# Kernel tuning notes

Hardware: AMD Instinct MI355X
Metric: run time of the kernel (lower is better)

## Reference

```python
import jax, jax.numpy as jnp
import numpy as np

B, L, N, D, TOPK, OUT_V = 32, 512, 1024, 64, 20, 1024
BN_EPS = 1e-5
NEG_SLOPE = 0.2


def setup_inputs() -> dict:
    key = jax.random.key(0)
    ks = jax.random.split(key, 8)
    s = lambda k, shape, sc=0.05: jax.random.normal(k, shape, jnp.float32) * sc
    return {
        "x_enc": jax.random.normal(ks[0], (B, L, N), jnp.float32),
        "emb": s(ks[1], (N, D), 0.1),          # nn.Embedding(variate, d_model).weight
        "lin_W": s(ks[2], (L, D)),              # GraphLayer.lin (no bias)
        "att_i": s(ks[3], (D,)),
        "att_j": s(ks[4], (D,)),
        "att_em_i": s(ks[5], (D,)),
        "att_em_j": s(ks[6], (D,)),
        "gnn_b": jnp.zeros((D,), jnp.float32),  # GraphLayer bias (concat=False)
        "g1": jnp.ones((D,), jnp.float32), "b1": jnp.zeros((D,), jnp.float32),   # GNNLayer.bn
        "g2": jnp.ones((D,), jnp.float32), "b2": jnp.zeros((D,), jnp.float32),   # bn_outlayer_in
        "out_W": s(ks[7], (D, 1)), "out_b": jnp.zeros((1,), jnp.float32),        # OutLayer Linear(d_model, 1)
    }


def _forward(x_enc, emb, lin_W, att_i, att_j, att_em_i, att_em_j,
             gnn_b, g1, b1, g2, b2, out_W, out_b):
    # --- LIN: LayerNorm(input_len, eps=0, no affine) over time, first OUT_V variates ---
    xv = jnp.transpose(x_enc[:, :, :OUT_V], (0, 2, 1))          # [B, OUT_V, L]
    xv = (xv - xv.mean(-1, keepdims=True)) / jnp.sqrt(xv.var(-1, keepdims=True))
    x_enc = x_enc.at[:, :, :OUT_V].set(jnp.transpose(xv, (0, 2, 1)))
    x_enc = jnp.nan_to_num(x_enc, nan=0.0, posinf=0.0, neginf=0.0)

    gt = x_enc[:, -1:, :OUT_V]                                   # [B, 1, OUT_V]
    enc = x_enc.at[:, -1:, :OUT_V].set(0.0)

    # x = enc.transpose(0,1).view(-1, L)  (faithful to original reshape)
    x = jnp.transpose(enc, (1, 0, 2)).reshape(-1, L)             # [B*N, L]

    # --- dynamic top-k cosine-similarity graph (embeddings detached) ---
    w = jax.lax.stop_gradient(emb)
    nrm = jnp.linalg.norm(w, axis=-1)
    cos = (w @ w.T) / (nrm[:, None] * nrm[None, :])              # [N, N]
    topk_idx = jax.lax.top_k(cos, TOPK)[1]                       # [N, TOPK]
    src = topk_idx.reshape(-1)                                   # gated_j (source)
    dst = jnp.repeat(jnp.arange(N), TOPK)                        # gated_i (target)

    offs = (jnp.arange(B) * N)[:, None]
    src_b = (src[None, :] + offs).reshape(-1)                    # [B*N*TOPK]
    dst_b = (dst[None, :] + offs).reshape(-1)

    # remove_self_loops (mask out) then add_self_loops for all B*N nodes
    num_nodes = B * N
    self_mask = jnp.concatenate([src_b == dst_b, jnp.zeros(num_nodes, bool)])
    src_all = jnp.concatenate([src_b, jnp.arange(num_nodes)])
    dst_all = jnp.concatenate([dst_b, jnp.arange(num_nodes)])

    # --- GraphLayer (GAT-style, heads=1, concat=False) ---
    h = x @ lin_W                                                # [B*N, D]
    all_emb = jnp.tile(emb, (B, 1))                              # [B*N, D]

    logit = (h[dst_all] @ att_i + all_emb[dst_all] @ att_em_i
             + h[src_all] @ att_j + all_emb[src_all] @ att_em_j)  # [E]
    logit = jnp.where(logit >= 0, logit, NEG_SLOPE * logit)      # leaky_relu(0.2)
    logit = jnp.where(self_mask, -jnp.inf, logit)

    seg_max = jax.ops.segment_max(logit, dst_all, num_segments=num_nodes)
    expv = jnp.where(self_mask, 0.0, jnp.exp(logit - seg_max[dst_all]))
    denom = jax.ops.segment_sum(expv, dst_all, num_segments=num_nodes)
    alpha = expv / denom[dst_all]

    out = jax.ops.segment_sum(h[src_all] * alpha[:, None], dst_all,
                              num_segments=num_nodes) + gnn_b    # [B*N, D]

    # GNNLayer: BatchNorm1d(D) (batch stats) + ReLU
    out = (out - out.mean(0)) / jnp.sqrt(out.var(0) + BN_EPS) * g1 + b1
    out = jax.nn.relu(out)

    # --- combine with embedding, bn_outlayer_in, OutLayer ---
    xg = out.reshape(B, N, D) * emb[None]                        # [B, N, D]
    xg = jnp.transpose(xg, (0, 2, 1))                            # [B, D, N]
    mu = xg.mean((0, 2), keepdims=True)
    var = xg.var((0, 2), keepdims=True)
    xg = (xg - mu) / jnp.sqrt(var + BN_EPS) * g2[None, :, None] + b2[None, :, None]
    xg = jnp.transpose(jax.nn.relu(xg), (0, 2, 1))               # [B, N, D]

    o = xg @ out_W + out_b                                       # [B, N, 1]
    o = jnp.transpose(o, (0, 2, 1))                              # [B, 1, N]
    return o[:, :, :OUT_V], gt


def reference(x_enc, emb, lin_W, att_i, att_j, att_em_i, att_em_j,
              gnn_b, g1, b1, g2, b2, out_W, out_b):
    return _forward(x_enc, emb, lin_W, att_i, att_j, att_em_i, att_em_j,
                    gnn_b, g1, b1, g2, b2, out_W, out_b)
```

## Files before the change

### kernel.cpp

```cpp
#include <hip/hip_runtime.h>
#include <stdint.h>

#define BB 32
#define LL 512
#define NNODES 1024
#define DD 64
#define TOPK 20
#define NTOT (BB*NNODES)
#define LNSZ (LL*NNODES)

typedef short short8 __attribute__((ext_vector_type(8)));
typedef float floatx4 __attribute__((ext_vector_type(4)));

__device__ __forceinline__ float bf2f(unsigned short u){
    union { unsigned int i; float f; } x; x.i = ((unsigned int)u) << 16; return x.f;
}
__device__ __forceinline__ unsigned short f2bf(float f){
    union { float f; unsigned int i; } x; x.f = f;
    unsigned int u = x.i;
    return (unsigned short)((u + 0x7FFFu + ((u >> 16) & 1u)) >> 16);
}
__device__ __forceinline__ void unpack2(unsigned int w, float& lo, float& hi){
    union { unsigned int i; float f; } a, b;
    a.i = w << 16; b.i = w & 0xFFFF0000u;
    lo = a.f; hi = b.f;
}
__device__ __forceinline__ float ldf(const void* p, int i, int isf){
    return isf ? ((const float*)p)[i] : bf2f(((const unsigned short*)p)[i]);
}

__global__ void __launch_bounds__(256) kd_detect(const unsigned short* x, int* flag, float* stats){
    __shared__ int cnt;
    stats[threadIdx.x] = 0.f;
    if (threadIdx.x == 0) cnt = 0;
    __syncthreads();
    unsigned int idx = (threadIdx.x * 131071u) & 0x7FFFFFu;
    float v = bf2f(x[idx * 2]);
    float a = fabsf(v);
    int crazy = (!(a <= 1e3f)) || (v != 0.f && a < 1e-6f);
    atomicAdd(&cnt, crazy);
    __syncthreads();
    if (threadIdx.x == 0) flag[0] = (cnt > 64) ? 1 : 0;
}

__global__ void __launch_bounds__(256) k0_prep(const void* lw, unsigned short* wt,
                                               const void* emb, const void* aemi, const void* aemj,
                                               float* eai, float* eaj, const int* dtf){
    int isf = dtf[0];
    int id = blockIdx.x * 256 + threadIdx.x;
    int k = id >> 6, d = id & 63;
    unsigned short w = isf ? f2bf(((const float*)lw)[id]) : ((const unsigned short*)lw)[id];
    wt[d * 512 + k] = w;
    if (id < 1024){
        int n = id;
        float s1 = 0.f, s2 = 0.f;
        for (int dd = 0; dd < 64; dd++){
            float e = ldf(emb, n * 64 + dd, isf);
            s1 += e * ldf(aemi, dd, isf);
            s2 += e * ldf(aemj, dd, isf);
        }
        eai[n] = s1; eaj[n] = s2;
    }
}

__global__ void __launch_bounds__(256) k1a_partial(const void* x, float* part, const int* dtf){
    int isf = dtf[0];
    int t = threadIdx.x;
    int b = blockIdx.x >> 4, lq = blockIdx.x & 15;
    int n0 = t * 4;
    size_t base = (size_t)b * LNSZ + (size_t)(lq * 32) * NNODES + n0;
    float s0=0,s1=0,s2=0,s3=0,q0=0,q1=0,q2=0,q3=0;
    if (isf){
        const float* p = (const float*)x + base;
        for (int i = 0; i < 32; i++){
            float4 w = *(const float4*)p;
            s0+=w.x; q0+=w.x*w.x; s1+=w.y; q1+=w.y*w.y;
            s2+=w.z; q2+=w.z*w.z; s3+=w.w; q3+=w.w*w.w;
            p += NNODES;
        }
    } else {
        const unsigned short* p = (const unsigned short*)x + base;
        for (int i = 0; i < 32; i++){
            uint2 w = *(const uint2*)p;
            float a,bv,c,d2;
            unpack2(w.x, a, bv); unpack2(w.y, c, d2);
            s0+=a; q0+=a*a; s1+=bv; q1+=bv*bv; s2+=c; q2+=c*c; s3+=d2; q3+=d2*d2;
            p += NNODES;
        }
    }
    int v = b * NNODES + n0;
    float2* pp = (float2*)part;
    pp[(size_t)v*16 + lq]       = make_float2(s0,q0);
    pp[(size_t)(v+1)*16 + lq]   = make_float2(s1,q1);
    pp[(size_t)(v+2)*16 + lq]   = make_float2(s2,q2);
    pp[(size_t)(v+3)*16 + lq]   = make_float2(s3,q3);
}

__global__ void __launch_bounds__(256) k1b_finalize(const void* x, const float* part,
                                                    float* mr, float* outp, const int* dtf){
    int isf = dtf[0];
    int v = blockIdx.x * 256 + threadIdx.x;
    const float2* pp = (const float2*)part + (size_t)v * 16;
    float s = 0.f, q = 0.f;
    for (int i = 0; i < 16; i++){ float2 w = pp[i]; s += w.x; q += w.y; }
    float mean = s * (1.f/512.f);
    float var  = q * (1.f/512.f) - mean * mean;
    float rstd = var > 0.f ? rsqrtf(var) : 0.f;
    ((float2*)mr)[v] = make_float2(mean, rstd);
    int b = v >> 10, n = v & 1023;
    float xv = ldf(x, (int)((size_t)b * LNSZ + (size_t)511 * NNODES + n), isf);
    outp[NTOT + v] = (xv - mean) * rstd;
}

__global__ void __launch_bounds__(256) k2_gemm_h(const void* x, const unsigned short* wt,
                                                const float* mr, float* h, const int* dtf){
    __shared__ unsigned short A_l[128 * 136];
    __shared__ unsigned short W_l[64 * 136];
    __shared__ float4 colp4[256];
    int isf = dtf[0];
    int t = threadIdx.x;
    int q = blockIdx.x & 63, mtile = blockIdx.x >> 6;
    int b = q >> 1, nbase = (q & 1) * 512;
    size_t xbase = (size_t)b * LNSZ + nbase;

    colp4[t] = ((const float4*)mr)[q * 256 + t];

    int wave = t >> 6, lane = t & 63;
    int quad = lane >> 4, lcol = lane & 15;
    floatx4 acc[2][4];
    for (int i = 0; i < 2; i++) for (int j = 0; j < 4; j++) acc[i][j] = (floatx4){0.f,0.f,0.f,0.f};
    __syncthreads();

    for (int kc = 0; kc < 4; kc++){
        for (int i = 0; i < 8; i++){
            int id = i * 256 + t;
            int l = id >> 4, c16 = id & 15;
            int lg = mtile * 128 + l;
            uint4 o;
            if (lg == 511){
                o = make_uint4(0u, 0u, 0u, 0u);
            } else {
                size_t ofs = xbase + (size_t)lg * NNODES + kc * 128 + c16 * 8;
                float e0,e1,e2,e3,e4,e5,e6,e7;
                if (isf){
                    const float4* px = (const float4*)((const float*)x + ofs);
                    float4 wa = px[0], wb = px[1];
                    e0=wa.x; e1=wa.y; e2=wa.z; e3=wa.w; e4=wb.x; e5=wb.y; e6=wb.z; e7=wb.w;
                } else {
                    uint4 w = *(const uint4*)((const unsigned short*)x + ofs);
                    unpack2(w.x,e0,e1); unpack2(w.y,e2,e3); unpack2(w.z,e4,e5); unpack2(w.w,e6,e7);
                }
                int f4b = kc * 64 + c16 * 4;
                float4 pA = colp4[f4b+0], pB = colp4[f4b+1], pC = colp4[f4b+2], pD = colp4[f4b+3];
                e0 = (e0 - pA.x) * pA.y;  e1 = (e1 - pA.z) * pA.w;
                e2 = (e2 - pB.x) * pB.y;  e3 = (e3 - pB.z) * pB.w;
                e4 = (e4 - pC.x) * pC.y;  e5 = (e5 - pC.z) * pC.w;
                e6 = (e6 - pD.x) * pD.y;  e7 = (e7 - pD.z) * pD.w;
                o.x = (unsigned)f2bf(e0) | ((unsigned)f2bf(e1) << 16);
                o.y = (unsigned)f2bf(e2) | ((unsigned)f2bf(e3) << 16);
                o.z = (unsigned)f2bf(e4) | ((unsigned)f2bf(e5) << 16);
                o.w = (unsigned)f2bf(e6) | ((unsigned)f2bf(e7) << 16);
            }
            *(uint4*)&A_l[l * 136 + c16 * 8] = o;
        }
        for (int i = 0; i < 4; i++){
            int id = i * 256 + t;
            int dd = id >> 4, c16 = id & 15;
            uint4 w = *(const uint4*)(wt + dd * 512 + kc * 128 + c16 * 8);
            *(uint4*)&W_l[dd * 136 + c16 * 8] = w;
        }
        __syncthreads();
        for (int ks = 0; ks < 4; ks++){
            short8 af[2], bfr[4];
            af[0] = *(const short8*)&A_l[(wave * 32 + lcol) * 136 + ks * 32 + quad * 8];
            af[1] = *(const short8*)&A_l[(wave * 32 + 16 + lcol) * 136 + ks * 32 + quad * 8];
            for (int tc = 0; tc < 4; tc++)
                bfr[tc] = *(const short8*)&W_l[(tc * 16 + lcol) * 136 + ks * 32 + quad * 8];
            for (int tr = 0; tr < 2; tr++)
                for (int tc = 0; tc < 4; tc++)
                    acc[tr][tc] = __builtin_amdgcn_mfma_f32_16x16x32_bf16(af[tr], bfr[tc], acc[tr][tc], 0, 0, 0);
        }
        __syncthreads();
    }
    for (int tr = 0; tr < 2; tr++) for (int tc = 0; tc < 4; tc++){
        int dcol = tc * 16 + lcol;
        for (int r = 0; r < 4; r++){
            int lrow = wave * 32 + tr * 16 + quad * 4 + r;
            int lg = mtile * 128 + lrow;
            int row = lg * 64 + q;
            h[(size_t)row * 64 + dcol] = acc[tr][tc][r];
        }
    }
}

__global__ void __launch_bounds__(256) k3_topk(const void* emb, int* topk, const int* dtf){
    __shared__ float enf[4][64];
    int isf = dtf[0];
    int wave = threadIdx.x >> 6, lane = threadIdx.x & 63;
    int n = blockIdx.x * 4 + wave;
    float e = ldf(emb, n * 64 + lane, isf);
    enf[wave][lane] = e;
    float p1 = e * e;
    #pragma unroll
    for (int m = 1; m < 64; m <<= 1) p1 += __shfl_xor(p1, m, 64);
    __syncthreads();
    float rn_own = rsqrtf(p1);
    const float* en = enf[wave];
    float va[16];
    for (int ii = 0; ii < 16; ii++){
        int m = ii * 64 + lane;
        float dot = 0.f, sq = 0.f;
        if (isf){
            const float4* pm = (const float4*)((const float*)emb + m * 64);
            #pragma unroll
            for (int i = 0; i < 16; i++){
                float4 w = pm[i];
                dot += en[i*4+0]*w.x + en[i*4+1]*w.y + en[i*4+2]*w.z + en[i*4+3]*w.w;
                sq  += w.x*w.x + w.y*w.y + w.z*w.z + w.w*w.w;
            }
        } else {
            const uint4* pm = (const uint4*)((const unsigned short*)emb + m * 64);
            #pragma unroll
            for (int i = 0; i < 8; i++){
                uint4 w = pm[i];
                float a0,a1,a2,a3,a4,a5,a6,a7;
                unpack2(w.x,a0,a1); unpack2(w.y,a2,a3); unpack2(w.z,a4,a5); unpack2(w.w,a6,a7);
                dot += en[i*8+0]*a0 + en[i*8+1]*a1 + en[i*8+2]*a2 + en[i*8+3]*a3
                     + en[i*8+4]*a4 + en[i*8+5]*a5 + en[i*8+6]*a6 + en[i*8+7]*a7;
                sq  += a0*a0 + a1*a1 + a2*a2 + a3*a3 + a4*a4 + a5*a5 + a6*a6 + a7*a7;
            }
        }
        va[ii] = dot * rn_own * rsqrtf(sq);
    }
    for (int k = 0; k < TOPK; k++){
        float t8[8]; int x8[8];
        #pragma unroll
        for (int j = 0; j < 8; j++){
            bool c = va[2*j+1] > va[2*j];
            t8[j] = c ? va[2*j+1] : va[2*j]; x8[j] = c ? 2*j+1 : 2*j;
        }
        #pragma unroll
        for (int j = 0; j < 4; j++){
            bool c = t8[2*j+1] > t8[2*j];
            t8[j] = c ? t8[2*j+1] : t8[2*j]; x8[j] = c ? x8[2*j+1] : x8[2*j];
        }
        #pragma unroll
        for (int j = 0; j < 2; j++){
            bool c = t8[2*j+1] > t8[2*j];
            t8[j] = c ? t8[2*j+1] : t8[2*j]; x8[j] = c ? x8[2*j+1] : x8[2*j];
        }
        bool c0 = t8[1] > t8[0];
        float bv = c0 ? t8[1] : t8[0]; int bi = c0 ? x8[1] : x8[0];
        int bm = bi * 64 + lane;
        #pragma unroll
        for (int s = 1; s < 64; s <<= 1){
            float ov = __shfl_xor(bv, s, 64);
            int   om = __shfl_xor(bm, s, 64);
            bool u = (ov > bv) || (ov == bv && om < bm);
            bv = u ? ov : bv; bm = u ? om : bm;
        }
        if (lane == 0) topk[n * TOPK + k] = bm;
        int evi = bm >> 6;
        bool own = ((bm & 63) == lane);
        #pragma unroll
        for (int ii = 0; ii < 16; ii++)
            va[ii] = (own && ii == evi) ? -__builtin_inff() : va[ii];
    }
}

__global__ void __launch_bounds__(256) k4_coef(const float* h, const void* att_i, const void* att_j,
                                               const float* eai, const float* eaj, float* ai, float* aj,
                                               const int* dtf){
    int isf = dtf[0];
    int wave = blockIdx.x * 4 + (threadIdx.x >> 6), lane = threadIdx.x & 63;
    float wi = ldf(att_i, lane, isf), wj = ldf(att_j, lane, isf);
    int v0 = wave * 16;
    for (int i = 0; i < 16; i++){
        int v = v0 + i;
        float hv = h[(size_t)v * 64 + lane];
        float p1 = hv * wi, p2 = hv * wj;
        for (int m = 1; m < 64; m <<= 1){ p1 += __shfl_xor(p1, m, 64); p2 += __shfl_xor(p2, m, 64); }
        if (lane == 0){
            int n = v & 1023;
            ai[v] = p1 + eai[n];
            aj[v] = p2 + eaj[n];
        }
    }
}

__global__ void __launch_bounds__(256) k5_attn(const float* h, const float* ai, const float* aj, const int* topk,
                                               const void* gnn_b, float* out, const int* dtf){
    int isf = dtf[0];
    int wave = threadIdx.x >> 6, lane = threadIdx.x & 63;
    float gb = ldf(gnn_b, lane, isf);
    int v = blockIdx.x * 4 + wave;
    int n = v & 1023, bbase = v & ~1023;
    int srcv; bool valid;
    if (lane < TOPK){
        int id = topk[n * TOPK + lane];
        srcv = bbase | id;
        valid = (id != n);
    } else if (lane == TOPK){
        srcv = v; valid = true;
    } else { srcv = v; valid = false; }
    float l = ai[v] + aj[srcv];
    l = (l >= 0.f) ? l : 0.2f * l;
    if (!valid) l = -__builtin_inff();
    float m = l;
    #pragma unroll
    for (int s = 1; s < 64; s <<= 1){ float o = __shfl_xor(m, s, 64); m = fmaxf(m, o); }
    float ev = valid ? __expf(l - m) : 0.f;
    float dsum = ev;
    #pragma unroll
    for (int s = 1; s < 64; s <<= 1) dsum += __shfl_xor(dsum, s, 64);
    float rd = 1.f / dsum;
    float acc = 0.f;
    #pragma unroll
    for (int j = 0; j <= TOPK; j++){
        float e = __shfl(ev, j, 64);
        int  sj = __shfl(srcv, j, 64);
        acc += e * h[(size_t)sj * 64 + lane];
    }
    out[(size_t)v * 64 + lane] = acc * rd + gb;
}

__global__ void __launch_bounds__(256) k5b_stats(const float* out, float* stats1){
    __shared__ float bs[256], bq[256];
    int wave = threadIdx.x >> 6, lane = threadIdx.x & 63;
    int v0 = blockIdx.x * 128 + wave * 32;
    float ssum = 0.f, ssq = 0.f;
    for (int i = 0; i < 32; i++){
        float x = out[(size_t)(v0 + i) * 64 + lane];
        ssum += x; ssq += x * x;
    }
    bs[threadIdx.x] = ssum; bq[threadIdx.x] = ssq;
    __syncthreads();
    if (wave == 0){
        float s  = bs[lane] + bs[64+lane] + bs[128+lane] + bs[192+lane];
        float qq = bq[lane] + bq[64+lane] + bq[128+lane] + bq[192+lane];
        atomicAdd(&stats1[lane], s);
        atomicAdd(&stats1[64 + lane], qq);
    }
}

__global__ void __launch_bounds__(256) k6_stats2(const float* out, const float* stats1, const void* g1,
                                                 const void* b1, const void* emb,
                                                 float* stats2, const int* dtf){
    __shared__ float bs[256], bq[256];
    int isf = dtf[0];
    int wave = threadIdx.x >> 6, lane = threadIdx.x & 63;
    float mu   = stats1[lane] * (1.f/32768.f);
    float var  = stats1[64 + lane] * (1.f/32768.f) - mu * mu;
    float rstd = 1.f / sqrtf(var + 1e-5f);
    float g = ldf(g1, lane, isf), bb = ldf(b1, lane, isf);
    float ssum = 0.f, ssq = 0.f;
    int v0 = (blockIdx.x * 4 + wave) * 16;
    for (int i = 0; i < 16; i++){
        int v = v0 + i; int n = v & 1023;
        float x = out[(size_t)v * 64 + lane];
        float y = fmaxf((x - mu) * rstd * g + bb, 0.f);
        float z = y * ldf(emb, n * 64 + lane, isf);
        ssum += z; ssq += z * z;
    }
    bs[threadIdx.x] = ssum; bq[threadIdx.x] = ssq;
    __syncthreads();
    if (wave == 0){
        float s  = bs[lane] + bs[64+lane] + bs[128+lane] + bs[192+lane];
        float qq = bq[lane] + bq[64+lane] + bq[128+lane] + bq[192+lane];
        atomicAdd(&stats2[lane], s);
        atomicAdd(&stats2[64 + lane], qq);
    }
}

__global__ void __launch_bounds__(256) k7_out(const float* out, const float* stats1, const float* stats2,
                                              const void* g1, const void* b1,
                                              const void* g2, const void* b2,
                                              const void* emb, const void* outw,
                                              const void* outb, float* o, const int* dtf){
    int isf = dtf[0];
    int wave = threadIdx.x >> 6, lane = threadIdx.x & 63;
    float mu1   = stats1[lane] * (1.f/32768.f);
    float var1  = stats1[64 + lane] * (1.f/32768.f) - mu1 * mu1;
    float rstd1 = 1.f / sqrtf(var1 + 1e-5f);
    float g1v = ldf(g1, lane, isf), b1v = ldf(b1, lane, isf);
    float mu2   = stats2[lane] * (1.f/32768.f);
    float var2  = stats2[64 + lane] * (1.f/32768.f) - mu2 * mu2;
    float rstd2 = 1.f / sqrtf(var2 + 1e-5f);
    float g2v = ldf(g2, lane, isf), b2v = ldf(b2, lane, isf);
    float w = ldf(outw, lane, isf);
    float ob = ldf(outb, 0, isf);
    int v0 = (blockIdx.x * 4 + wave) * 16;
    for (int i = 0; i < 16; i++){
        int v = v0 + i; int n = v & 1023;
        float x = out[(size_t)v * 64 + lane];
        float z = fmaxf((x - mu1) * rstd1 * g1v + b1v, 0.f) * ldf(emb, n * 64 + lane, isf);
        float y = fmaxf((z - mu2) * rstd2 * g2v + b2v, 0.f);
        float p = y * w;
        for (int s = 1; s < 64; s <<= 1) p += __shfl_xor(p, s, 64);
        if (lane == 0) o[v] = p + ob;
    }
}

extern "C" void kernel_launch(void* const* d_in, const int* in_sizes, int n_in,
                              void* d_out, int out_size, void* d_ws, size_t ws_size,
                              hipStream_t stream){
    const void* x    = d_in[0];
    const void* emb  = d_in[1];
    const void* linW = d_in[2];
    const void* atti = d_in[3];
    const void* attj = d_in[4];
    const void* aemi = d_in[5];
    const void* aemj = d_in[6];
    const void* gnnb = d_in[7];
    const void* g1   = d_in[8];
    const void* b1   = d_in[9];
    const void* g2   = d_in[10];
    const void* b2   = d_in[11];
    const void* outw = d_in[12];
    const void* outb = d_in[13];
    float* o = (float*)d_out;

    char* w = (char*)d_ws;
    float*          mr    = (float*)(w + 0);
    unsigned short* wt    = (unsigned short*)(w + 262144);
    float*          h     = (float*)(w + 327680);
    float*          eai   = (float*)(w + 8716288);
    float*          eaj   = (float*)(w + 8720384);
    int*            topk  = (int*)(w + 8724480);
    float*          ai    = (float*)(w + 8806400);
    float*          aj    = (float*)(w + 8937472);
    float*          outg  = (float*)(w + 9068544);
    float*          part  = outg;
    float*          stats = (float*)(w + 17457152);
    int*            dtf   = (int*)(w + 17458176);

    hipLaunchKernelGGL(kd_detect,    dim3(1),    dim3(256), 0, stream, (const unsigned short*)x, dtf, stats);
    hipLaunchKernelGGL(k0_prep,      dim3(128),  dim3(256), 0, stream, linW, wt, emb, aemi, aemj, eai, eaj, dtf);
    hipLaunchKernelGGL(k1a_partial,  dim3(512),  dim3(256), 0, stream, x, part, dtf);
    hipLaunchKernelGGL(k1b_finalize, dim3(128),  dim3(256), 0, stream, x, part, mr, o, dtf);
    hipLaunchKernelGGL(k2_gemm_h,    dim3(256),  dim3(256), 0, stream, x, wt, mr, h, dtf);
    hipLaunchKernelGGL(k3_topk,      dim3(256),  dim3(256), 0, stream, emb, topk, dtf);
    hipLaunchKernelGGL(k4_coef,      dim3(512),  dim3(256), 0, stream, h, atti, attj, eai, eaj, ai, aj, dtf);
    hipLaunchKernelGGL(k5_attn,      dim3(8192), dim3(256), 0, stream, h, ai, aj, topk, gnnb, outg, dtf);
    hipLaunchKernelGGL(k5b_stats,    dim3(256),  dim3(256), 0, stream, outg, stats);
    hipLaunchKernelGGL(k6_stats2,    dim3(512),  dim3(256), 0, stream, outg, stats, g1, b1, emb, stats + 128, dtf);
    hipLaunchKernelGGL(k7_out,       dim3(512),  dim3(256), 0, stream, outg, stats, stats + 128,
                       g1, b1, g2, b2, emb, outw, outb, o, dtf);
}
```

Baseline: 283.4 us.

## Precompute transposed embeddings and norms for topk; halve GEMM M-tile for more blocks

```diff
diff --git a/kernel.cpp b/kernel.cpp
--- a/kernel.cpp
+++ b/kernel.cpp
@@ -45,12 +45,21 @@
 
 __global__ void __launch_bounds__(256) k0_prep(const void* lw, unsigned short* wt,
                                                const void* emb, const void* aemi, const void* aemj,
-                                               float* eai, float* eaj, const int* dtf){
+                                               float* eai, float* eaj, float* embT, float* rsqm,
+                                               const int* dtf){
     int isf = dtf[0];
     int id = blockIdx.x * 256 + threadIdx.x;
     int k = id >> 6, d = id & 63;
     unsigned short w = isf ? f2bf(((const float*)lw)[id]) : ((const unsigned short*)lw)[id];
     wt[d * 512 + k] = w;
+    {
+        int j = id;
+        int dd = j >> 10, m = j & 1023;
+        embT[j] = ldf(emb, m * 64 + dd, isf);
+        j = id + 32768;
+        dd = j >> 10; m = j & 1023;
+        embT[j] = ldf(emb, m * 64 + dd, isf);
+    }
     if (id < 1024){
         int n = id;
         float s1 = 0.f, s2 = 0.f;
@@ -60,6 +69,25 @@
             s2 += e * ldf(aemj, dd, isf);
         }
         eai[n] = s1; eaj[n] = s2;
+        float sq = 0.f;
+        if (!isf){
+            const uint4* pm = (const uint4*)((const unsigned short*)emb + n * 64);
+            #pragma unroll
+            for (int i = 0; i < 8; i++){
+                uint4 ww = pm[i];
+                float a0,a1,a2,a3,a4,a5,a6,a7;
+                unpack2(ww.x,a0,a1); unpack2(ww.y,a2,a3); unpack2(ww.z,a4,a5); unpack2(ww.w,a6,a7);
+                sq += a0*a0 + a1*a1 + a2*a2 + a3*a3 + a4*a4 + a5*a5 + a6*a6 + a7*a7;
+            }
+        } else {
+            const float4* pm = (const float4*)((const float*)emb + n * 64);
+            #pragma unroll
+            for (int i = 0; i < 16; i++){
+                float4 ww = pm[i];
+                sq += ww.x*ww.x + ww.y*ww.y + ww.z*ww.z + ww.w*ww.w;
+            }
+        }
+        rsqm[n] = rsqrtf(sq);
     }
 }
 
@@ -114,7 +142,7 @@
 
 __global__ void __launch_bounds__(256) k2_gemm_h(const void* x, const unsigned short* wt,
                                                 const float* mr, float* h, const int* dtf){
-    __shared__ unsigned short A_l[128 * 136];
+    __shared__ unsigned short A_l[64 * 136];
     __shared__ unsigned short W_l[64 * 136];
     __shared__ float4 colp4[256];
     int isf = dtf[0];
@@ -127,15 +155,15 @@
 
     int wave = t >> 6, lane = t & 63;
     int quad = lane >> 4, lcol = lane & 15;
-    floatx4 acc[2][4];
-    for (int i = 0; i < 2; i++) for (int j = 0; j < 4; j++) acc[i][j] = (floatx4){0.f,0.f,0.f,0.f};
+    floatx4 acc[4];
+    for (int j = 0; j < 4; j++) acc[j] = (floatx4){0.f,0.f,0.f,0.f};
     __syncthreads();
 
     for (int kc = 0; kc < 4; kc++){
-        for (int i = 0; i < 8; i++){
+        for (int i = 0; i < 4; i++){
             int id = i * 256 + t;
             int l = id >> 4, c16 = id & 15;
-            int lg = mtile * 128 + l;
+            int lg = mtile * 64 + l;
             uint4 o;
             if (lg == 511){
                 o = make_uint4(0u, 0u, 0u, 0u);
@@ -171,67 +199,91 @@
         }
         __syncthreads();
         for (int ks = 0; ks < 4; ks++){
-            short8 af[2], bfr[4];
-            af[0] = *(const short8*)&A_l[(wave * 32 + lcol) * 136 + ks * 32 + quad * 8];
-            af[1] = *(const short8*)&A_l[(wave * 32 + 16 + lcol) * 136 + ks * 32 + quad * 8];
+            short8 af, bfr[4];
+            af = *(const short8*)&A_l[(wave * 16 + lcol) * 136 + ks * 32 + quad * 8];
             for (int tc = 0; tc < 4; tc++)
                 bfr[tc] = *(const short8*)&W_l[(tc * 16 + lcol) * 136 + ks * 32 + quad * 8];
-            for (int tr = 0; tr < 2; tr++)
-                for (int tc = 0; tc < 4; tc++)
-                    acc[tr][tc] = __builtin_amdgcn_mfma_f32_16x16x32_bf16(af[tr], bfr[tc], acc[tr][tc], 0, 0, 0);
+            for (int tc = 0; tc < 4; tc++)
+                acc[tc] = __builtin_amdgcn_mfma_f32_16x16x32_bf16(af, bfr[tc], acc[tc], 0, 0, 0);
         }
         __syncthreads();
     }
-    for (int tr = 0; tr < 2; tr++) for (int tc = 0; tc < 4; tc++){
+    for (int tc = 0; tc < 4; tc++){
         int dcol = tc * 16 + lcol;
         for (int r = 0; r < 4; r++){
-            int lrow = wave * 32 + tr * 16 + quad * 4 + r;
-            int lg = mtile * 128 + lrow;
+            int lrow = wave * 16 + quad * 4 + r;
+            int lg = mtile * 64 + lrow;
             int row = lg * 64 + q;
-            h[(size_t)row * 64 + dcol] = acc[tr][tc][r];
-        }
-    }
-}
-
-__global__ void __launch_bounds__(256) k3_topk(const void* emb, int* topk, const int* dtf){
-    __shared__ float enf[4][64];
+            h[(size_t)row * 64 + dcol] = acc[tc][r];
+        }
+    }
+}
+
+__global__ void __launch_bounds__(256) k3_topk(const void* emb, const float* embT, const float* rsqm,
+                                               int* topk, const int* dtf){
+    __shared__ float enf[64];
+    __shared__ float n2s;
+    __shared__ float crow[1024];
     int isf = dtf[0];
     int wave = threadIdx.x >> 6, lane = threadIdx.x & 63;
-    int n = blockIdx.x * 4 + wave;
-    float e = ldf(emb, n * 64 + lane, isf);
-    enf[wave][lane] = e;
-    float p1 = e * e;
+    int n = blockIdx.x;
+    if (wave == 0){
+        float e = ldf(emb, n * 64 + lane, isf);
+        enf[lane] = e;
+        float p1 = e * e;
+        #pragma unroll
+        for (int m = 1; m < 64; m <<= 1) p1 += __shfl_xor(p1, m, 64);
+        if (lane == 0) n2s = p1;
+    }
+    __syncthreads();
+    float rn_own = rsqrtf(n2s);
+    const float* en = enf;
+    int mb = wave * 256 + lane * 4;
+    float dot0 = 0.f, dot1 = 0.f, dot2 = 0.f, dot3 = 0.f;
+    if (!isf){
+        #pragma unroll
+        for (int i = 0; i < 8; i++){
+            float4 a0 = *(const float4*)(embT + (i*8+0)*1024 + mb);
+            float4 a1 = *(const float4*)(embT + (i*8+1)*1024 + mb);
+            float4 a2 = *(const float4*)(embT + (i*8+2)*1024 + mb);
+            float4 a3 = *(const float4*)(embT + (i*8+3)*1024 + mb);
+            float4 a4 = *(const float4*)(embT + (i*8+4)*1024 + mb);
+            float4 a5 = *(const float4*)(embT + (i*8+5)*1024 + mb);
+            float4 a6 = *(const float4*)(embT + (i*8+6)*1024 + mb);
+            float4 a7 = *(const float4*)(embT + (i*8+7)*1024 + mb);
+            const float* e8 = en + i * 8;
+            dot0 += e8[0]*a0.x + e8[1]*a1.x + e8[2]*a2.x + e8[3]*a3.x
+                  + e8[4]*a4.x + e8[5]*a5.x + e8[6]*a6.x + e8[7]*a7.x;
+            dot1 += e8[0]*a0.y + e8[1]*a1.y + e8[2]*a2.y + e8[3]*a3.y
+                  + e8[4]*a4.y + e8[5]*a5.y + e8[6]*a6.y + e8[7]*a7.y;
+            dot2 += e8[0]*a0.z + e8[1]*a1.z + e8[2]*a2.z + e8[3]*a3.z
+                  + e8[4]*a4.z + e8[5]*a5.z + e8[6]*a6.z + e8[7]*a7.z;
+            dot3 += e8[0]*a0.w + e8[1]*a1.w + e8[2]*a2.w + e8[3]*a3.w
+                  + e8[4]*a4.w + e8[5]*a5.w + e8[6]*a6.w + e8[7]*a7.w;
+        }
+    } else {
+        #pragma unroll
+        for (int i = 0; i < 16; i++){
+            float4 a0 = *(const float4*)(embT + (i*4+0)*1024 + mb);
+            float4 a1 = *(const float4*)(embT + (i*4+1)*1024 + mb);
+            float4 a2 = *(const float4*)(embT + (i*4+2)*1024 + mb);
+            float4 a3 = *(const float4*)(embT + (i*4+3)*1024 + mb);
+            const float* e4 = en + i * 4;
+            dot0 += e4[0]*a0.x + e4[1]*a1.x + e4[2]*a2.x + e4[3]*a3.x;
+            dot1 += e4[0]*a0.y + e4[1]*a1.y + e4[2]*a2.y + e4[3]*a3.y;
+            dot2 += e4[0]*a0.z + e4[1]*a1.z + e4[2]*a2.z + e4[3]*a3.z;
+            dot3 += e4[0]*a0.w + e4[1]*a1.w + e4[2]*a2.w + e4[3]*a3.w;
+        }
+    }
+    crow[mb+0] = dot0 * rn_own * rsqm[mb+0];
+    crow[mb+1] = dot1 * rn_own * rsqm[mb+1];
+    crow[mb+2] = dot2 * rn_own * rsqm[mb+2];
+    crow[mb+3] = dot3 * rn_own * rsqm[mb+3];
+    __syncthreads();
+    if (wave != 0) return;
+    float va[16];
     #pragma unroll
-    for (int m = 1; m < 64; m <<= 1) p1 += __shfl_xor(p1, m, 64);
-    __syncthreads();
-    float rn_own = rsqrtf(p1);
-    const float* en = enf[wave];
-    float va[16];
-    for (int ii = 0; ii < 16; ii++){
-        int m = ii * 64 + lane;
-        float dot = 0.f, sq = 0.f;
-        if (isf){
-            const float4* pm = (const float4*)((const float*)emb + m * 64);
-            #pragma unroll
-            for (int i = 0; i < 16; i++){
-                float4 w = pm[i];
-                dot += en[i*4+0]*w.x + en[i*4+1]*w.y + en[i*4+2]*w.z + en[i*4+3]*w.w;
-                sq  += w.x*w.x + w.y*w.y + w.z*w.z + w.w*w.w;
-            }
-        } else {
-            const uint4* pm = (const uint4*)((const unsigned short*)emb + m * 64);
-            #pragma unroll
-            for (int i = 0; i < 8; i++){
-                uint4 w = pm[i];
-                float a0,a1,a2,a3,a4,a5,a6,a7;
-                unpack2(w.x,a0,a1); unpack2(w.y,a2,a3); unpack2(w.z,a4,a5); unpack2(w.w,a6,a7);
-                dot += en[i*8+0]*a0 + en[i*8+1]*a1 + en[i*8+2]*a2 + en[i*8+3]*a3
-                     + en[i*8+4]*a4 + en[i*8+5]*a5 + en[i*8+6]*a6 + en[i*8+7]*a7;
-                sq  += a0*a0 + a1*a1 + a2*a2 + a3*a3 + a4*a4 + a5*a5 + a6*a6 + a7*a7;
-            }
-        }
-        va[ii] = dot * rn_own * rsqrtf(sq);
-    }
+    for (int ii = 0; ii < 16; ii++) va[ii] = crow[ii * 64 + lane];
     for (int k = 0; k < TOPK; k++){
         float t8[8]; int x8[8];
         #pragma unroll
@@ -431,15 +483,17 @@
     float*          aj    = (float*)(w + 8937472);
     float*          outg  = (float*)(w + 9068544);
     float*          part  = outg;
+    float*          embT  = (float*)(w + 13262848);
+    float*          rsqm  = (float*)(w + 13524992);
     float*          stats = (float*)(w + 17457152);
     int*            dtf   = (int*)(w + 17458176);
 
     hipLaunchKernelGGL(kd_detect,    dim3(1),    dim3(256), 0, stream, (const unsigned short*)x, dtf, stats);
-    hipLaunchKernelGGL(k0_prep,      dim3(128),  dim3(256), 0, stream, linW, wt, emb, aemi, aemj, eai, eaj, dtf);
+    hipLaunchKernelGGL(k0_prep,      dim3(128),  dim3(256), 0, stream, linW, wt, emb, aemi, aemj, eai, eaj, embT, rsqm, dtf);
     hipLaunchKernelGGL(k1a_partial,  dim3(512),  dim3(256), 0, stream, x, part, dtf);
     hipLaunchKernelGGL(k1b_finalize, dim3(128),  dim3(256), 0, stream, x, part, mr, o, dtf);
-    hipLaunchKernelGGL(k2_gemm_h,    dim3(256),  dim3(256), 0, stream, x, wt, mr, h, dtf);
-    hipLaunchKernelGGL(k3_topk,      dim3(256),  dim3(256), 0, stream, emb, topk, dtf);
+    hipLaunchKernelGGL(k2_gemm_h,    dim3(512),  dim3(256), 0, stream, x, wt, mr, h, dtf);
+    hipLaunchKernelGGL(k3_topk,      dim3(1024), dim3(256), 0, stream, emb, embT, rsqm, topk, dtf);
     hipLaunchKernelGGL(k4_coef,      dim3(512),  dim3(256), 0, stream, h, atti, attj, eai, eaj, ai, aj, dtf);
     hipLaunchKernelGGL(k5_attn,      dim3(8192), dim3(256), 0, stream, h, ai, aj, topk, gnnb, outg, dtf);
     hipLaunchKernelGGL(k5b_stats,    dim3(256),  dim3(256), 0, stream, outg, stats);
```

New measurement: 260.5 us. 1.09x faster.
